# Optimization experiments

Hardware: AMD Instinct MI355X
Metric: run time of the kernel (lower is better)

Reference implementation:

```python
import jax, jax.numpy as jnp
import numpy as np

NEG_BIG = 1e9  # additive mask magnitude from the original code


def setup_inputs() -> dict:
    key = jax.random.key(0)
    k1, k2, k3 = jax.random.split(key, 3)
    B, H, W, Cqk, Cv = 4, 64, 64, 256, 256
    return {
        "query": jax.random.normal(k1, (B, H, W, Cqk), dtype=jnp.float32),
        "key": jax.random.normal(k2, (B, H, W, Cqk), dtype=jnp.float32),
        "value": jax.random.normal(k3, (B, H, W, Cv), dtype=jnp.float32),
    }


def reference(query, key, value):
    B = query.shape[0]
    Cqk = key.shape[-1]
    Cv = value.shape[-1]
    out_spatial = query.shape[1:-1]

    q = query.reshape(B, -1, Cqk)   # [B, Sq, C]
    k = key.reshape(B, -1, Cqk)     # [B, S, C]
    v = value.reshape(B, -1, Cv)    # [B, S, Cv]
    Sq = q.shape[1]

    # PixelSNAIL causal mask: position i may attend to strictly earlier
    # positions j < i (row 0 attends to nothing -> zero output row).
    allowed = jnp.tril(jnp.ones((Sq, Sq), dtype=q.dtype), k=-1)  # [Sq, S]

    scale = 1.0 / jnp.sqrt(jnp.asarray(Cqk, dtype=q.dtype))
    scores = jnp.einsum("bqc,bkc->bqk", q, k) * scale  # [B, Sq, S]
    scores = scores - NEG_BIG * (1.0 - allowed)
    probs = jax.nn.softmax(scores, axis=-1) * allowed   # zero out masked probs
    mixed = jnp.einsum("bqk,bkv->bqv", probs, v)        # [B, Sq, Cv]
    return mixed.reshape((B,) + out_spatial + (Cv,))
```

## Files before the change

kernel.cpp:

```cpp
#include <hip/hip_runtime.h>

#define S_LEN 4096
#define DIM   256
#define QBLK  128
#define KVBLK 64
#define TILE_SH (KVBLK * DIM)
#define PER_B  1056
#define NBLK   256

typedef __attribute__((ext_vector_type(4))) float f32x4;
typedef __attribute__((ext_vector_type(8))) short bf16x8;
typedef __attribute__((ext_vector_type(4))) unsigned short u16x4;
typedef __attribute__((ext_vector_type(8))) unsigned short u16x8;

__device__ __forceinline__ unsigned short f2bf(float x) {
    union { float f; unsigned u; } v; v.f = x;
    unsigned r = v.u + 0x7FFFu + ((v.u >> 16) & 1u);
    return (unsigned short)(r >> 16);
}
__device__ __forceinline__ float bf2f(unsigned short h) {
    union { unsigned u; float f; } v; v.u = ((unsigned)h) << 16;
    return v.f;
}

__device__ __forceinline__ void g2l16(const unsigned short* g, unsigned short* s) {
    __builtin_amdgcn_global_load_lds(
        (const __attribute__((address_space(1))) unsigned int*)g,
        (__attribute__((address_space(3))) unsigned int*)s, 16, 0, 0);
}

__device__ __forceinline__ void decode_item(int x, int& b, int& qt, int& t) {
    b = x / PER_B;
    int r = x - b * PER_B;
    int q = (int)((__fsqrt_rn(4.0f * (float)r + 1.0f) - 1.0f) * 0.5f);
    while ((q + 1) * (q + 2) <= r) ++q;
    while (q * (q + 1) > r) --q;
    qt = q;
    t = r - q * (q + 1);
}

__global__ __launch_bounds__(256) void prepass(
        const float* __restrict__ K, const float* __restrict__ V,
        unsigned short* __restrict__ KW, unsigned short* __restrict__ VW) {
    __shared__ unsigned short vt[TILE_SH];
    const int tile = blockIdx.x;
    const int tid  = threadIdx.x;
    const float* ks = K + (size_t)tile * (KVBLK * DIM);
    const float* vs = V + (size_t)tile * (KVBLK * DIM);

    char* kw = (char*)(KW + (size_t)tile * TILE_SH);
#pragma unroll
    for (int j = 0; j < 8; ++j) {
        int u = j * 256 + tid;
        int row = u >> 5, c8 = u & 31;
        f32x4 a  = *(const f32x4*)(ks + row * DIM + c8 * 8);
        f32x4 bb = *(const f32x4*)(ks + row * DIM + c8 * 8 + 4);
        u16x8 h;
        h[0] = f2bf(a[0]);  h[1] = f2bf(a[1]);  h[2] = f2bf(a[2]);  h[3] = f2bf(a[3]);
        h[4] = f2bf(bb[0]); h[5] = f2bf(bb[1]); h[6] = f2bf(bb[2]); h[7] = f2bf(bb[3]);
        unsigned off = (unsigned)(row * 512 + c8 * 16) ^ (unsigned)((row & 7) << 4);
        *(u16x8*)(kw + off) = h;
    }
    {
        int col = tid;
#pragma unroll
        for (int r8 = 0; r8 < 8; ++r8) {
            u16x8 h;
#pragma unroll
            for (int e = 0; e < 8; ++e) h[e] = f2bf(vs[(r8 * 8 + e) * DIM + col]);
            unsigned off = (unsigned)(col * 128 + r8 * 16) ^ (unsigned)((col & 7) << 4);
            *(u16x8*)((char*)vt + off) = h;
        }
    }
    __syncthreads();
    char* vw = (char*)(VW + (size_t)tile * TILE_SH);
#pragma unroll
    for (int j = 0; j < 8; ++j) {
        int u = j * 256 + tid;
        *(u16x8*)(vw + u * 16) = *(const u16x8*)((const char*)vt + u * 16);
    }
}

template<bool PACKED>
__global__ __launch_bounds__(512, 1) void attn_flash(
        const float* __restrict__ Qg, const unsigned short* __restrict__ KW,
        const unsigned short* __restrict__ VW, unsigned short* __restrict__ OP,
        float* __restrict__ ML, float* __restrict__ Og) {
    __shared__ unsigned short Ksh[2][TILE_SH];
    __shared__ unsigned short VshT[2][TILE_SH];
    __shared__ unsigned short Psh[8][16 * KVBLK];

    const int tid = threadIdx.x;
    const int w   = tid >> 6;
    const int l   = tid & 63;
    const int l15 = l & 15;
    const int lg  = l >> 4;

    int s, e;
    if (PACKED) {
        const int i = blockIdx.x;
        s = (33 * i) >> 1;
        e = (33 * (i + 1)) >> 1;
    } else {
        const int b0 = blockIdx.x & 3, q0 = blockIdx.x >> 2;
        s = b0 * PER_B + q0 * (q0 + 1);
        e = s + 2 * q0 + 2;
    }

    int b, qt, t;
    decode_item(s, b, qt, t);
    int tstart = t;
    bool firstSec = true;

    bf16x8 qf[8];
    {
        const float* qp = Qg + (size_t)(b * S_LEN + qt * QBLK + w * 16 + l15) * DIM + lg * 8;
#pragma unroll
        for (int ks = 0; ks < 8; ++ks) {
            f32x4 a = *(const f32x4*)(qp + ks * 32);
            f32x4 c = *(const f32x4*)(qp + ks * 32 + 4);
            bf16x8 f;
            f[0] = (short)f2bf(a[0] * 0.0625f); f[1] = (short)f2bf(a[1] * 0.0625f);
            f[2] = (short)f2bf(a[2] * 0.0625f); f[3] = (short)f2bf(a[3] * 0.0625f);
            f[4] = (short)f2bf(c[0] * 0.0625f); f[5] = (short)f2bf(c[1] * 0.0625f);
            f[6] = (short)f2bf(c[2] * 0.0625f); f[7] = (short)f2bf(c[3] * 0.0625f);
            qf[ks] = f;
        }
    }

    f32x4 acc[16];
#pragma unroll
    for (int i = 0; i < 16; ++i) acc[i] = (f32x4)0.0f;
    float mrun = -1e30f, lrun = 0.f;

    {
        const unsigned short* kimg = KW + (size_t)(b * 64 + t) * TILE_SH + w * 2048 + l * 8;
        const unsigned short* vimg = VW + (size_t)(b * 64 + t) * TILE_SH + w * 2048 + l * 8;
        unsigned short* kd = &Ksh[0][w * 2048];
        unsigned short* vd = &VshT[0][w * 2048];
#pragma unroll
        for (int i = 0; i < 4; ++i) {
            g2l16(kimg + i * 512, kd + i * 512);
            g2l16(vimg + i * 512, vd + i * 512);
        }
    }
    __syncthreads();

    int x = s, cur = 0;
    while (true) {
        const bool have_next = (x + 1 < e);
        int nb = b, nqt = qt, ntt = t + 1;
        const bool secEnd = !have_next || (ntt >= 2 * qt + 2);
        if (have_next) {
            if (ntt >= 2 * qt + 2) decode_item(x + 1, nb, nqt, ntt);
            const unsigned short* kimg = KW + (size_t)(nb * 64 + ntt) * TILE_SH + w * 2048 + l * 8;
            const unsigned short* vimg = VW + (size_t)(nb * 64 + ntt) * TILE_SH + w * 2048 + l * 8;
            unsigned short* kd = &Ksh[cur ^ 1][w * 2048];
            unsigned short* vd = &VshT[cur ^ 1][w * 2048];
#pragma unroll
            for (int i = 0; i < 4; ++i) {
                g2l16(kimg + i * 512, kd + i * 512);
                g2l16(vimg + i * 512, vd + i * 512);
            }
        }

        const int wqlo = qt * QBLK + w * 16;
        const bool skip = (t * KVBLK >= wqlo + 16);
        const bool msk  = (t * KVBLK + KVBLK - 1 >= wqlo);

        if (!skip) {
            f32x4 sacc[4];
#pragma unroll
            for (int j = 0; j < 4; ++j) sacc[j] = (f32x4)0.0f;
#pragma unroll
            for (int ks = 0; ks < 8; ++ks) {
#pragma unroll
                for (int jt = 0; jt < 4; ++jt) {
                    int j = jt * 16 + l15;
                    unsigned off = (unsigned)(j * 512 + (ks * 32 + lg * 8) * 2);
                    off ^= (unsigned)((j & 7) << 4);
                    bf16x8 kb = *(const bf16x8*)((const char*)Ksh[cur] + off);
                    sacc[jt] = __builtin_amdgcn_mfma_f32_16x16x32_bf16(kb, qf[ks], sacc[jt], 0, 0, 0);
                }
            }
            if (msk) {
                const int qg = wqlo + l15;
#pragma unroll
                for (int jt = 0; jt < 4; ++jt)
#pragma unroll
                    for (int rr = 0; rr < 4; ++rr) {
                        int kg = t * KVBLK + jt * 16 + lg * 4 + rr;
                        if (kg >= qg) sacc[jt][rr] = -3e38f;
                    }
            }
            {
                float m0 = fmaxf(fmaxf(sacc[0][0], sacc[0][1]), fmaxf(sacc[0][2], sacc[0][3]));
                float m1 = fmaxf(fmaxf(sacc[1][0], sacc[1][1]), fmaxf(sacc[1][2], sacc[1][3]));
                float m2 = fmaxf(fmaxf(sacc[2][0], sacc[2][1]), fmaxf(sacc[2][2], sacc[2][3]));
                float m3 = fmaxf(fmaxf(sacc[3][0], sacc[3][1]), fmaxf(sacc[3][2], sacc[3][3]));
                float mx = fmaxf(fmaxf(m0, m1), fmaxf(m2, m3));
                mx = fmaxf(mx, __shfl_xor(mx, 16));
                mx = fmaxf(mx, __shfl_xor(mx, 32));
                float mnew = fmaxf(mrun, mx);
                float corr = __expf(mrun - mnew);
                mrun = mnew;
                float ls = 0.f;
#pragma unroll
                for (int jt = 0; jt < 4; ++jt)
#pragma unroll
                    for (int rr = 0; rr < 4; ++rr) {
                        float p = __expf(sacc[jt][rr] - mnew);
                        sacc[jt][rr] = p;
                        ls += p;
                    }
                ls += __shfl_xor(ls, 16);
                ls += __shfl_xor(ls, 32);
                lrun = lrun * corr + ls;
#pragma unroll
                for (int nt = 0; nt < 16; ++nt) acc[nt] *= corr;
            }
            {
                char* pw = (char*)&Psh[w][0];
                unsigned base = (unsigned)(l15 * 128 + lg * 8) ^ (unsigned)((l15 & 7) << 4);
#pragma unroll
                for (int jt = 0; jt < 4; ++jt) {
                    u16x4 pk;
                    pk.x = f2bf(sacc[jt][0]); pk.y = f2bf(sacc[jt][1]);
                    pk.z = f2bf(sacc[jt][2]); pk.w = f2bf(sacc[jt][3]);
                    *(u16x4*)(pw + (base ^ (unsigned)(jt * 32))) = pk;
                }
            }
#pragma unroll
            for (int ks = 0; ks < 2; ++ks) {
                unsigned poff = (unsigned)(l15 * 128 + ks * 64 + lg * 16);
                poff ^= (unsigned)((l15 & 7) << 4);
                bf16x8 pb = *(const bf16x8*)((const char*)&Psh[w][0] + poff);
#pragma unroll
                for (int nt = 0; nt < 16; ++nt) {
                    unsigned voff = (unsigned)((nt * 16 + l15) * 128 + ks * 64 + lg * 16);
                    voff ^= (unsigned)((l15 & 7) << 4);
                    bf16x8 va = *(const bf16x8*)((const char*)VshT[cur] + voff);
                    acc[nt] = __builtin_amdgcn_mfma_f32_16x16x32_bf16(va, pb, acc[nt], 0, 0, 0);
                }
            }
        }
        __syncthreads();

        if (secEnd) {
            const bool complete = (tstart == 0) && (t == 2 * qt + 1);
            if (complete) {
                float rl = (lrun > 0.f) ? (1.0f / lrun) : 0.f;
                float* ob = Og + (size_t)(b * S_LEN + wqlo + l15) * DIM;
#pragma unroll
                for (int nt = 0; nt < 16; ++nt) {
                    f32x4 o = acc[nt] * rl;
                    *(f32x4*)(ob + nt * 16 + lg * 4) = o;
                }
            } else {
                const int slot = 2 * blockIdx.x + (firstSec ? 0 : 1);
                unsigned short* op = OP + (size_t)slot * (QBLK * DIM)
                                        + (size_t)(w * 16 + l15) * DIM;
#pragma unroll
                for (int nt = 0; nt < 16; ++nt) {
                    u16x4 ph;
                    ph.x = f2bf(acc[nt][0]); ph.y = f2bf(acc[nt][1]);
                    ph.z = f2bf(acc[nt][2]); ph.w = f2bf(acc[nt][3]);
                    *(u16x4*)(op + nt * 16 + lg * 4) = ph;
                }
                if (lg == 0) {
                    float* mlp = ML + (size_t)slot * (2 * QBLK);
                    mlp[(w * 16 + l15) * 2]     = mrun;
                    mlp[(w * 16 + l15) * 2 + 1] = lrun;
                }
            }
            if (!have_next) break;
            {
                const float* qp = Qg + (size_t)(nb * S_LEN + nqt * QBLK + w * 16 + l15) * DIM + lg * 8;
#pragma unroll
                for (int ks = 0; ks < 8; ++ks) {
                    f32x4 a = *(const f32x4*)(qp + ks * 32);
                    f32x4 c = *(const f32x4*)(qp + ks * 32 + 4);
                    bf16x8 f;
                    f[0] = (short)f2bf(a[0] * 0.0625f); f[1] = (short)f2bf(a[1] * 0.0625f);
                    f[2] = (short)f2bf(a[2] * 0.0625f); f[3] = (short)f2bf(a[3] * 0.0625f);
                    f[4] = (short)f2bf(c[0] * 0.0625f); f[5] = (short)f2bf(c[1] * 0.0625f);
                    f[6] = (short)f2bf(c[2] * 0.0625f); f[7] = (short)f2bf(c[3] * 0.0625f);
                    qf[ks] = f;
                }
            }
#pragma unroll
            for (int i = 0; i < 16; ++i) acc[i] = (f32x4)0.0f;
            mrun = -1e30f; lrun = 0.f;
            firstSec = false; tstart = 0;
        }
        ++x; b = nb; qt = nqt; t = ntt; cur ^= 1;
    }
}

__global__ __launch_bounds__(256) void attn_combine(
        const unsigned short* __restrict__ OP, const float* __restrict__ ML,
        float* __restrict__ Og) {
    const int id = blockIdx.x;
    const int rg = id & 3;
    const int bq = id >> 2;
    const int b  = bq >> 5;
    const int qt = bq & 31;
    const int A  = b * PER_B + qt * (qt + 1);
    const int E  = A + 2 * qt + 2;
    const int j0 = (2 * A + 1) / 33;
    const int j1 = (2 * E - 1) / 33;
    if (j0 >= j1) return;
    const int C = j1 - j0 + 1;

    int slots[6];
    for (int c = 0; c < C; ++c) {
        int j  = j0 + c;
        int sj = (33 * j) >> 1;
        slots[c] = 2 * j + ((sj >= A) ? 0 : 1);
    }

    const int tid = threadIdx.x;
    float* outb = Og + ((size_t)(b * S_LEN + qt * QBLK)) * DIM;
#pragma unroll
    for (int jj = 0; jj < 4; ++jj) {
        int u   = jj * 256 + tid;
        int row = rg * 32 + (u >> 5);
        int d8  = u & 31;
        float M = -1e30f;
        for (int c = 0; c < C; ++c)
            M = fmaxf(M, ML[(size_t)slots[c] * (2 * QBLK) + row * 2]);
        float L = 0.f;
        float o[8];
#pragma unroll
        for (int e2 = 0; e2 < 8; ++e2) o[e2] = 0.f;
        for (int c = 0; c < C; ++c) {
            float mm = ML[(size_t)slots[c] * (2 * QBLK) + row * 2];
            float ll = ML[(size_t)slots[c] * (2 * QBLK) + row * 2 + 1];
            float sc = __expf(mm - M);
            L += ll * sc;
            u16x8 ph = *(const u16x8*)(OP + ((size_t)slots[c] * QBLK + row) * DIM + d8 * 8);
#pragma unroll
            for (int e2 = 0; e2 < 8; ++e2) o[e2] += sc * bf2f(ph[e2]);
        }
        float rl = (L > 0.f) ? (1.0f / L) : 0.f;
        f32x4 o0, o1;
        o0[0] = o[0] * rl; o0[1] = o[1] * rl; o0[2] = o[2] * rl; o0[3] = o[3] * rl;
        o1[0] = o[4] * rl; o1[1] = o[5] * rl; o1[2] = o[6] * rl; o1[3] = o[7] * rl;
        *(f32x4*)(outb + (size_t)row * DIM + d8 * 8)     = o0;
        *(f32x4*)(outb + (size_t)row * DIM + d8 * 8 + 4) = o1;
    }
}

extern "C" void kernel_launch(void* const* d_in, const int* in_sizes, int n_in,
                              void* d_out, int out_size, void* d_ws, size_t ws_size,
                              hipStream_t stream) {
    const float* q = (const float*)d_in[0];
    const float* k = (const float*)d_in[1];
    const float* v = (const float*)d_in[2];
    float* o = (float*)d_out;

    const size_t imgShorts = (size_t)256 * TILE_SH;
    const size_t IMG = 2 * imgShorts * sizeof(unsigned short);
    unsigned short* KW = (unsigned short*)d_ws;
    unsigned short* VW = KW + imgShorts;

    const int nslots = 2 * NBLK;
    const size_t need = IMG
        + (size_t)nslots * (QBLK * DIM) * 2
        + (size_t)nslots * (2 * QBLK) * 4;
    if (ws_size < IMG) return;

    hipLaunchKernelGGL(prepass, dim3(256), dim3(256), 0, stream, k, v, KW, VW);
    if (ws_size >= need) {
        unsigned short* OP = (unsigned short*)((char*)d_ws + IMG);
        float* ML = (float*)(OP + (size_t)nslots * (QBLK * DIM));
        hipLaunchKernelGGL((attn_flash<true>), dim3(NBLK), dim3(512), 0, stream,
                           q, KW, VW, OP, ML, o);
        hipLaunchKernelGGL(attn_combine, dim3(512), dim3(256), 0, stream,
                           OP, ML, o);
    } else {
        hipLaunchKernelGGL((attn_flash<false>), dim3(128), dim3(512), 0, stream,
                           q, KW, VW, (unsigned short*)nullptr, (float*)nullptr, o);
    }
}
```

Before: 108.0 us.

## Drop online max tracking and pair waves to share V fragments across two query groups

```diff
diff --git a/kernel.cpp b/kernel.cpp
--- a/kernel.cpp
+++ b/kernel.cpp
@@ -7,6 +7,7 @@
 #define TILE_SH (KVBLK * DIM)
 #define PER_B  1056
 #define NBLK   256
+#define TOT    4224
 
 typedef __attribute__((ext_vector_type(4))) float f32x4;
 typedef __attribute__((ext_vector_type(8))) short bf16x8;
@@ -89,12 +90,16 @@
     __shared__ unsigned short Ksh[2][TILE_SH];
     __shared__ unsigned short VshT[2][TILE_SH];
     __shared__ unsigned short Psh[8][16 * KVBLK];
+    __shared__ float lsh[8][16];
 
     const int tid = threadIdx.x;
     const int w   = tid >> 6;
     const int l   = tid & 63;
     const int l15 = l & 15;
     const int lg  = l >> 4;
+    const int p   = w >> 1;
+    const int h   = w & 1;
+    const int qga = 2 * p, qgb = 2 * p + 1;
 
     int s, e;
     if (PACKED) {
@@ -128,10 +133,12 @@
         }
     }
 
-    f32x4 acc[16];
-#pragma unroll
-    for (int i = 0; i < 16; ++i) acc[i] = (f32x4)0.0f;
-    float mrun = -1e30f, lrun = 0.f;
+    f32x4 acc[2][8];
+#pragma unroll
+    for (int qi = 0; qi < 2; ++qi)
+#pragma unroll
+        for (int i2 = 0; i2 < 8; ++i2) acc[qi][i2] = (f32x4)0.0f;
+    float lrun = 0.f;
 
     {
         const unsigned short* kimg = KW + (size_t)(b * 64 + t) * TILE_SH + w * 2048 + l * 8;
@@ -164,14 +171,17 @@
             }
         }
 
-        const int wqlo = qt * QBLK + w * 16;
-        const bool skip = (t * KVBLK >= wqlo + 16);
-        const bool msk  = (t * KVBLK + KVBLK - 1 >= wqlo);
-
-        if (!skip) {
+        const int qbase  = qt * QBLK;
+        const bool skipq  = (t * KVBLK >= qbase + w * 16 + 16);
+        const bool skippv = (t * KVBLK >= qbase + qgb * 16 + 16);
+        const bool mskq   = (t * KVBLK + KVBLK - 1 >= qbase + w * 16);
+
+        u16x4 pk[4];
+        if (!skipq) {
             f32x4 sacc[4];
 #pragma unroll
             for (int j = 0; j < 4; ++j) sacc[j] = (f32x4)0.0f;
+            __builtin_amdgcn_s_setprio(1);
 #pragma unroll
             for (int ks = 0; ks < 8; ++ks) {
 #pragma unroll
@@ -183,8 +193,9 @@
                     sacc[jt] = __builtin_amdgcn_mfma_f32_16x16x32_bf16(kb, qf[ks], sacc[jt], 0, 0, 0);
                 }
             }
-            if (msk) {
-                const int qg = wqlo + l15;
+            __builtin_amdgcn_s_setprio(0);
+            if (mskq) {
+                const int qg = qbase + w * 16 + l15;
 #pragma unroll
                 for (int jt = 0; jt < 4; ++jt)
 #pragma unroll
@@ -193,83 +204,95 @@
                         if (kg >= qg) sacc[jt][rr] = -3e38f;
                     }
             }
-            {
-                float m0 = fmaxf(fmaxf(sacc[0][0], sacc[0][1]), fmaxf(sacc[0][2], sacc[0][3]));
-                float m1 = fmaxf(fmaxf(sacc[1][0], sacc[1][1]), fmaxf(sacc[1][2], sacc[1][3]));
-                float m2 = fmaxf(fmaxf(sacc[2][0], sacc[2][1]), fmaxf(sacc[2][2], sacc[2][3]));
-                float m3 = fmaxf(fmaxf(sacc[3][0], sacc[3][1]), fmaxf(sacc[3][2], sacc[3][3]));
-                float mx = fmaxf(fmaxf(m0, m1), fmaxf(m2, m3));
-                mx = fmaxf(mx, __shfl_xor(mx, 16));
-                mx = fmaxf(mx, __shfl_xor(mx, 32));
-                float mnew = fmaxf(mrun, mx);
-                float corr = __expf(mrun - mnew);
-                mrun = mnew;
-                float ls = 0.f;
-#pragma unroll
-                for (int jt = 0; jt < 4; ++jt)
-#pragma unroll
-                    for (int rr = 0; rr < 4; ++rr) {
-                        float p = __expf(sacc[jt][rr] - mnew);
-                        sacc[jt][rr] = p;
-                        ls += p;
-                    }
-                ls += __shfl_xor(ls, 16);
-                ls += __shfl_xor(ls, 32);
-                lrun = lrun * corr + ls;
-#pragma unroll
-                for (int nt = 0; nt < 16; ++nt) acc[nt] *= corr;
-            }
-            {
-                char* pw = (char*)&Psh[w][0];
-                unsigned base = (unsigned)(l15 * 128 + lg * 8) ^ (unsigned)((l15 & 7) << 4);
-#pragma unroll
-                for (int jt = 0; jt < 4; ++jt) {
-                    u16x4 pk;
-                    pk.x = f2bf(sacc[jt][0]); pk.y = f2bf(sacc[jt][1]);
-                    pk.z = f2bf(sacc[jt][2]); pk.w = f2bf(sacc[jt][3]);
-                    *(u16x4*)(pw + (base ^ (unsigned)(jt * 32))) = pk;
-                }
-            }
+            float ls = 0.f;
+#pragma unroll
+            for (int jt = 0; jt < 4; ++jt) {
+                f32x4 pv;
+#pragma unroll
+                for (int rr = 0; rr < 4; ++rr) {
+                    float pe = __expf(sacc[jt][rr]);
+                    pv[rr] = pe;
+                    ls += pe;
+                }
+                pk[jt].x = f2bf(pv[0]); pk[jt].y = f2bf(pv[1]);
+                pk[jt].z = f2bf(pv[2]); pk[jt].w = f2bf(pv[3]);
+            }
+            ls += __shfl_xor(ls, 16);
+            ls += __shfl_xor(ls, 32);
+            lrun += ls;
+        } else {
+#pragma unroll
+            for (int jt = 0; jt < 4; ++jt) { pk[jt].x = 0; pk[jt].y = 0; pk[jt].z = 0; pk[jt].w = 0; }
+        }
+        {
+            char* pw = (char*)&Psh[w][0];
+            unsigned base = (unsigned)(l15 * 128 + lg * 8) ^ (unsigned)((l15 & 7) << 4);
+#pragma unroll
+            for (int jt = 0; jt < 4; ++jt)
+                *(u16x4*)(pw + (base ^ (unsigned)(jt * 32))) = pk[jt];
+        }
+        __syncthreads();
+
+        if (!skippv) {
+            __builtin_amdgcn_s_setprio(1);
 #pragma unroll
             for (int ks = 0; ks < 2; ++ks) {
                 unsigned poff = (unsigned)(l15 * 128 + ks * 64 + lg * 16);
                 poff ^= (unsigned)((l15 & 7) << 4);
-                bf16x8 pb = *(const bf16x8*)((const char*)&Psh[w][0] + poff);
-#pragma unroll
-                for (int nt = 0; nt < 16; ++nt) {
+                bf16x8 pa_ = *(const bf16x8*)((const char*)&Psh[qga][0] + poff);
+                bf16x8 pb_ = *(const bf16x8*)((const char*)&Psh[qgb][0] + poff);
+#pragma unroll
+                for (int ni = 0; ni < 8; ++ni) {
+                    int nt = h * 8 + ni;
                     unsigned voff = (unsigned)((nt * 16 + l15) * 128 + ks * 64 + lg * 16);
                     voff ^= (unsigned)((l15 & 7) << 4);
                     bf16x8 va = *(const bf16x8*)((const char*)VshT[cur] + voff);
-                    acc[nt] = __builtin_amdgcn_mfma_f32_16x16x32_bf16(va, pb, acc[nt], 0, 0, 0);
-                }
-            }
+                    acc[0][ni] = __builtin_amdgcn_mfma_f32_16x16x32_bf16(va, pa_, acc[0][ni], 0, 0, 0);
+                    acc[1][ni] = __builtin_amdgcn_mfma_f32_16x16x32_bf16(va, pb_, acc[1][ni], 0, 0, 0);
+                }
+            }
+            __builtin_amdgcn_s_setprio(0);
         }
         __syncthreads();
 
         if (secEnd) {
+            if (lg == 0) lsh[w][l15] = lrun;
+            __syncthreads();
             const bool complete = (tstart == 0) && (t == 2 * qt + 1);
             if (complete) {
-                float rl = (lrun > 0.f) ? (1.0f / lrun) : 0.f;
-                float* ob = Og + (size_t)(b * S_LEN + wqlo + l15) * DIM;
-#pragma unroll
-                for (int nt = 0; nt < 16; ++nt) {
-                    f32x4 o = acc[nt] * rl;
-                    *(f32x4*)(ob + nt * 16 + lg * 4) = o;
+                float la = lsh[qga][l15], lb = lsh[qgb][l15];
+                float rla = (la > 0.f) ? (1.0f / la) : 0.f;
+                float rlb = (lb > 0.f) ? (1.0f / lb) : 0.f;
+                float* oa = Og + (size_t)(b * S_LEN + qbase + qga * 16 + l15) * DIM;
+                float* ob = Og + (size_t)(b * S_LEN + qbase + qgb * 16 + l15) * DIM;
+#pragma unroll
+                for (int ni = 0; ni < 8; ++ni) {
+                    int nt = h * 8 + ni;
+                    f32x4 o0 = acc[0][ni] * rla;
+                    f32x4 o1 = acc[1][ni] * rlb;
+                    *(f32x4*)(oa + nt * 16 + lg * 4) = o0;
+                    *(f32x4*)(ob + nt * 16 + lg * 4) = o1;
                 }
             } else {
                 const int slot = 2 * blockIdx.x + (firstSec ? 0 : 1);
-                unsigned short* op = OP + (size_t)slot * (QBLK * DIM)
-                                        + (size_t)(w * 16 + l15) * DIM;
-#pragma unroll
-                for (int nt = 0; nt < 16; ++nt) {
-                    u16x4 ph;
-                    ph.x = f2bf(acc[nt][0]); ph.y = f2bf(acc[nt][1]);
-                    ph.z = f2bf(acc[nt][2]); ph.w = f2bf(acc[nt][3]);
-                    *(u16x4*)(op + nt * 16 + lg * 4) = ph;
+                unsigned short* opa = OP + (size_t)slot * (QBLK * DIM)
+                                         + (size_t)(qga * 16 + l15) * DIM;
+                unsigned short* opb = OP + (size_t)slot * (QBLK * DIM)
+                                         + (size_t)(qgb * 16 + l15) * DIM;
+#pragma unroll
+                for (int ni = 0; ni < 8; ++ni) {
+                    int nt = h * 8 + ni;
+                    u16x4 pa2, pb2;
+                    pa2.x = f2bf(acc[0][ni][0]); pa2.y = f2bf(acc[0][ni][1]);
+                    pa2.z = f2bf(acc[0][ni][2]); pa2.w = f2bf(acc[0][ni][3]);
+                    pb2.x = f2bf(acc[1][ni][0]); pb2.y = f2bf(acc[1][ni][1]);
+                    pb2.z = f2bf(acc[1][ni][2]); pb2.w = f2bf(acc[1][ni][3]);
+                    *(u16x4*)(opa + nt * 16 + lg * 4) = pa2;
+                    *(u16x4*)(opb + nt * 16 + lg * 4) = pb2;
                 }
                 if (lg == 0) {
                     float* mlp = ML + (size_t)slot * (2 * QBLK);
-                    mlp[(w * 16 + l15) * 2]     = mrun;
+                    mlp[(w * 16 + l15) * 2]     = 0.0f;
                     mlp[(w * 16 + l15) * 2 + 1] = lrun;
                 }
             }
@@ -289,8 +312,10 @@
                 }
             }
 #pragma unroll
-            for (int i = 0; i < 16; ++i) acc[i] = (f32x4)0.0f;
-            mrun = -1e30f; lrun = 0.f;
+            for (int qi = 0; qi < 2; ++qi)
+#pragma unroll
+                for (int i2 = 0; i2 < 8; ++i2) acc[qi][i2] = (f32x4)0.0f;
+            lrun = 0.f;
             firstSec = false; tstart = 0;
         }
         ++x; b = nb; qt = nqt; t = ntt; cur ^= 1;
```

Result: faster. 101.5 us (-5.9%).
